# Kernel tuning notes

Hardware: AMD Instinct MI355X
Metric: run time of the kernel (lower is better)

## Reference

```python
import math
import jax, jax.numpy as jnp
import numpy as np

B, S, H, D = 8, 2048, 16, 80
DM = H * D  # 1280 = input_dims


def setup_inputs() -> dict:
    key = jax.random.key(0)
    ks = jax.random.split(key, 10)
    s = 0.02
    return {
        "x": jax.random.normal(ks[0], (B, S, DM), dtype=jnp.float32),
        "Wq": jax.random.normal(ks[1], (DM, DM), dtype=jnp.float32) * s,
        "bq": jnp.zeros((DM,), dtype=jnp.float32),
        "Wk": jax.random.normal(ks[2], (DM, DM), dtype=jnp.float32) * s,
        "bk": jnp.zeros((DM,), dtype=jnp.float32),
        "Wv": jax.random.normal(ks[3], (DM, DM), dtype=jnp.float32) * s,
        "bv": jnp.zeros((DM,), dtype=jnp.float32),
        "Wp": jax.random.normal(ks[4], (DM, DM), dtype=jnp.float32) * s,
        "bp": jnp.zeros((DM,), dtype=jnp.float32),
        "per_dim_scale": jnp.ones((D,), dtype=jnp.float32),
    }


def reference(x, Wq, bq, Wk, bk, Wv, bv, Wp, bp, per_dim_scale):
    # Projections: [B,S,DM] -> [B,S,H,D]
    q = (x @ Wq + bq).reshape(B, S, H, D)
    k = (x @ Wk + bk).reshape(B, S, H, D)
    v = (x @ Wv + bv).reshape(B, S, H, D)
    # Faithful to source: matmul over last two dims of (B,S,H,D) tensors,
    # i.e. scores are [B,S,H,H] -- mixing across HEADS at each position.
    scale = 1.0 / math.sqrt(D)
    attn = jnp.einsum('bshd,bstd->bsht', q, k) * scale  # [B,S,H,H]
    attn = jax.nn.softmax(attn, axis=-1)
    out = jnp.einsum('bsht,bstd->bshd', attn, v)  # [B,S,H,D]
    out = out * per_dim_scale  # broadcast over D
    out = out.reshape(B, S, DM)
    return out @ Wp + bp
```

## Files before the change

### kernel.cpp

```cpp
#include <hip/hip_runtime.h>
#include <hip/hip_bf16.h>

#define M_TOT   16384
#define DMODEL  1280
#define NHEAD   16
#define DHEAD   80
#define NTC     5
#define BK      64
#define NKT     (DMODEL / BK)

typedef __attribute__((ext_vector_type(8))) __bf16 bf16x8;
typedef __attribute__((ext_vector_type(4))) float  f32x4;

__device__ __forceinline__ void gload16(const void* g, void* l) {
  __builtin_amdgcn_global_load_lds(
      (const __attribute__((address_space(1))) void*)g,
      (__attribute__((address_space(3))) void*)l, 16, 0, 0);
}

__device__ __forceinline__ float bf2f(unsigned short u) {
  return __uint_as_float((unsigned)u << 16);
}

__global__ __launch_bounds__(256) void cvt_bf16_kernel(
    const float* __restrict__ x, __hip_bfloat16* __restrict__ y, int n4) {
  int i = blockIdx.x * 256 + threadIdx.x;
  if (i >= n4) return;
  float4 v = ((const float4*)x)[i];
  union { ushort4 u; __hip_bfloat16 h[4]; } o;
  o.h[0] = __float2bfloat16(v.x);
  o.h[1] = __float2bfloat16(v.y);
  o.h[2] = __float2bfloat16(v.z);
  o.h[3] = __float2bfloat16(v.w);
  ((ushort4*)y)[i] = o.u;
}

__global__ __launch_bounds__(256) void transpose_cvt_kernel(
    const float* __restrict__ W0, const float* __restrict__ W1,
    const float* __restrict__ W2, const float* __restrict__ W3,
    const float* __restrict__ pds,
    __hip_bfloat16* __restrict__ T0, __hip_bfloat16* __restrict__ T1,
    __hip_bfloat16* __restrict__ T2, __hip_bfloat16* __restrict__ T3) {
  const float* W = blockIdx.z == 0 ? W0 : blockIdx.z == 1 ? W1
                 : blockIdx.z == 2 ? W2 : W3;
  __hip_bfloat16* T = blockIdx.z == 0 ? T0 : blockIdx.z == 1 ? T1
                    : blockIdx.z == 2 ? T2 : T3;
  __shared__ float tile[32][33];
  int bx = blockIdx.x * 32, by = blockIdx.y * 32;
  int tx = threadIdx.x, ty = threadIdx.y;
  for (int j = 0; j < 32; j += 8)
    tile[ty + j][tx] = W[(size_t)(by + ty + j) * DMODEL + bx + tx];
  __syncthreads();
  const float scale = (blockIdx.z == 3) ? pds[(by + tx) % DHEAD] : 1.0f;
  for (int j = 0; j < 32; j += 8)
    T[(size_t)(bx + ty + j) * DMODEL + by + tx] =
        __float2bfloat16(tile[tx][ty + j] * scale);
}

#define MFMA16(AF, BF, MB)                                                   \
  do {                                                                       \
    _Pragma("unroll")                                                        \
    for (int j_ = 0; j_ < 4; ++j_) {                                         \
      _Pragma("unroll")                                                      \
      for (int n_ = 0; n_ < 4; ++n_)                                         \
        acc[(MB) + j_][n_] = __builtin_amdgcn_mfma_f32_16x16x32_bf16(        \
            AF[j_], BF[n_], acc[(MB) + j_][n_], 0, 0, 0);                    \
    }                                                                        \
  } while (0)

template <bool OUT_BF16>
__global__ __launch_bounds__(512, 2) void gemm_bt_kernel(
    const __hip_bfloat16* __restrict__ A,
    const __hip_bfloat16* __restrict__ Bt0,
    const __hip_bfloat16* __restrict__ Bt1,
    const __hip_bfloat16* __restrict__ Bt2,
    const float* __restrict__ bias0, const float* __restrict__ bias1,
    const float* __restrict__ bias2,
    void* __restrict__ C0, void* __restrict__ C1, void* __restrict__ C2) {
  const int mat   = blockIdx.y / NTC;
  const int ntile = blockIdx.y % NTC;
  const __hip_bfloat16* Bt = mat == 0 ? Bt0 : mat == 1 ? Bt1 : Bt2;
  const float* bias        = mat == 0 ? bias0 : mat == 1 ? bias1 : bias2;
  void* C                  = mat == 0 ? C0 : mat == 1 ? C1 : C2;

  const int bm = blockIdx.x * 256;
  const int bn = ntile * 256;

  __shared__ __align__(16) char SLDS[131072];

  const int tid  = threadIdx.x;
  const int lane = tid & 63;
  const int wid  = tid >> 6;
  const int wm   = (wid >> 2) * 128;
  const int wn   = (wid & 3) * 64;
  const int lrow = lane & 15;
  const int l4   = lane >> 4;

  const int rsub  = lane >> 2;
  const int cswz  = (lane & 3) ^ ((rsub >> 1) & 3);
  const char* gsrc[2][2][2];
#pragma unroll
  for (int i = 0; i < 2; ++i) {
    const int rA = bm + wid * 32 + i * 16 + rsub;
    const int rB = bn + wid * 32 + i * 16 + rsub;
#pragma unroll
    for (int s = 0; s < 2; ++s) {
      gsrc[0][i][s] = (const char*)A  + (size_t)rA * (DMODEL * 2) + s * 64 + cswz * 16;
      gsrc[1][i][s] = (const char*)Bt + (size_t)rB * (DMODEL * 2) + s * 64 + cswz * 16;
    }
  }

  auto issueGroup = [&](int M, int s, int nbuf, size_t koff) {
    char* d = SLDS + M * 65536 + nbuf * 32768 + s * 16384 + wid * 2048;
    gload16(gsrc[M][0][s] + koff, d);
    gload16(gsrc[M][1][s] + koff, d + 1024);
  };

  f32x4 acc[8][4];
#pragma unroll
  for (int i = 0; i < 8; ++i)
#pragma unroll
    for (int j = 0; j < 4; ++j) acc[i][j] = (f32x4){0.f, 0.f, 0.f, 0.f};

  const int swz  = ((l4 ^ ((lrow >> 1) & 3)) << 4);
  const int aOff = (wm + lrow) * 64 + swz;
  const int bOff = 65536 + (wn + lrow) * 64 + swz;

  issueGroup(0, 0, 0, 0);
  issueGroup(1, 0, 0, 0);
  issueGroup(0, 1, 0, 0);
  issueGroup(1, 1, 0, 0);
  asm volatile("s_waitcnt vmcnt(4)" ::: "memory");
  __builtin_amdgcn_s_barrier();

  bf16x8 aFa[4], aFb[4], aFc[4], aFd[4], bF0[4], bF1[4];
#pragma unroll
  for (int j = 0; j < 4; ++j)
    aFa[j] = *(const bf16x8*)(const void*)(SLDS + aOff + j * 1024);
#pragma unroll
  for (int n = 0; n < 4; ++n)
    bF0[n] = *(const bf16x8*)(const void*)(SLDS + bOff + n * 1024);
#pragma unroll
  for (int j = 0; j < 4; ++j)
    aFb[j] = *(const bf16x8*)(const void*)(SLDS + aOff + (4 + j) * 1024);

  for (int t = 0; t < NKT; ++t) {
    const int buf = t & 1, nbuf = buf ^ 1;
    const int b0 = buf << 15;
    const int n0 = nbuf << 15;
    const size_t koff = (size_t)(t + 1) * (BK * 2);
    const bool pf = (t + 1 < NKT);

    if (pf) {
      issueGroup(0, 0, nbuf, koff);
      asm volatile("s_waitcnt vmcnt(2)" ::: "memory");
    } else {
      asm volatile("s_waitcnt vmcnt(0)" ::: "memory");
    }
    __builtin_amdgcn_s_barrier();
#pragma unroll
    for (int j = 0; j < 4; ++j)
      aFc[j] = *(const bf16x8*)(const void*)(SLDS + b0 + 16384 + aOff + j * 1024);
#pragma unroll
    for (int n = 0; n < 4; ++n)
      bF1[n] = *(const bf16x8*)(const void*)(SLDS + b0 + 16384 + bOff + n * 1024);
#pragma unroll
    for (int j = 0; j < 4; ++j)
      aFd[j] = *(const bf16x8*)(const void*)(SLDS + b0 + 16384 + aOff + (4 + j) * 1024);
    if (pf) issueGroup(1, 0, nbuf, koff);
    __builtin_amdgcn_s_setprio(1);
    MFMA16(aFa, bF0, 0);
    MFMA16(aFb, bF0, 4);
    __builtin_amdgcn_s_setprio(0);

    if (pf) {
      issueGroup(0, 1, nbuf, koff);
      asm volatile("s_waitcnt vmcnt(2)" ::: "memory");
      __builtin_amdgcn_s_barrier();
#pragma unroll
      for (int j = 0; j < 4; ++j)
        aFa[j] = *(const bf16x8*)(const void*)(SLDS + n0 + aOff + j * 1024);
#pragma unroll
      for (int n = 0; n < 4; ++n)
        bF0[n] = *(const bf16x8*)(const void*)(SLDS + n0 + bOff + n * 1024);
#pragma unroll
      for (int j = 0; j < 4; ++j)
        aFb[j] = *(const bf16x8*)(const void*)(SLDS + n0 + aOff + (4 + j) * 1024);
      issueGroup(1, 1, nbuf, koff);
    }
    __builtin_amdgcn_s_setprio(1);
    MFMA16(aFc, bF1, 0);
    MFMA16(aFd, bF1, 4);
    __builtin_amdgcn_s_setprio(0);
  }

  const int rbase = l4 * 4;
#pragma unroll
  for (int mi = 0; mi < 8; ++mi) {
#pragma unroll
    for (int ni = 0; ni < 4; ++ni) {
      const int col = bn + wn + ni * 16 + lrow;
      const float b2 = bias[col];
#pragma unroll
      for (int r = 0; r < 4; ++r) {
        const int row = bm + wm + mi * 16 + rbase + r;
        const float val = acc[mi][ni][r] + b2;
        if (OUT_BF16)
          ((__hip_bfloat16*)C)[(size_t)row * DMODEL + col] = __float2bfloat16(val);
        else
          ((float*)C)[(size_t)row * DMODEL + col] = val;
      }
    }
  }
}

__global__ __launch_bounds__(256, 2) void gemm_bt128_kernel(
    const __hip_bfloat16* __restrict__ A,
    const __hip_bfloat16* __restrict__ Bt,
    const float* __restrict__ bias,
    float* __restrict__ C) {
  const int bm = blockIdx.x * 128;
  const int bn = blockIdx.y * 128;

  __shared__ __align__(16) char SLDS[65536];

  const int tid  = threadIdx.x;
  const int lane = tid & 63;
  const int wid  = tid >> 6;
  const int wm   = (wid >> 1) * 64;
  const int wn   = (wid & 1) * 64;
  const int lrow = lane & 15;
  const int l4   = lane >> 4;

  const int rsub  = lane >> 2;
  const int cswz  = (lane & 3) ^ ((rsub >> 1) & 3);
  const char* gsrc[2][2][2];
#pragma unroll
  for (int i = 0; i < 2; ++i) {
    const int rA = bm + wid * 32 + i * 16 + rsub;
    const int rB = bn + wid * 32 + i * 16 + rsub;
#pragma unroll
    for (int s = 0; s < 2; ++s) {
      gsrc[0][i][s] = (const char*)A  + (size_t)rA * (DMODEL * 2) + s * 64 + cswz * 16;
      gsrc[1][i][s] = (const char*)Bt + (size_t)rB * (DMODEL * 2) + s * 64 + cswz * 16;
    }
  }

  auto issueGroup = [&](int M, int s, int nbuf, size_t koff) {
    char* d = SLDS + M * 32768 + nbuf * 16384 + s * 8192 + wid * 2048;
    gload16(gsrc[M][0][s] + koff, d);
    gload16(gsrc[M][1][s] + koff, d + 1024);
  };

  f32x4 acc[4][4];
#pragma unroll
  for (int i = 0; i < 4; ++i)
#pragma unroll
    for (int j = 0; j < 4; ++j) acc[i][j] = (f32x4){0.f, 0.f, 0.f, 0.f};

  const int swz  = ((l4 ^ ((lrow >> 1) & 3)) << 4);
  const int aOff = (wm + lrow) * 64 + swz;
  const int bOff = 32768 + (wn + lrow) * 64 + swz;

  issueGroup(0, 0, 0, 0);
  issueGroup(1, 0, 0, 0);
  issueGroup(0, 1, 0, 0);
  issueGroup(1, 1, 0, 0);

  for (int t = 0; t < NKT; ++t) {
    const int buf = t & 1, nbuf = buf ^ 1;
    const int b0 = buf << 14;
    const size_t koff = (size_t)(t + 1) * (BK * 2);
    const bool pf = (t + 1 < NKT);

    asm volatile("s_waitcnt vmcnt(4)" ::: "memory");
    __builtin_amdgcn_s_barrier();
    bf16x8 aF[4], bF[4];
#pragma unroll
    for (int j = 0; j < 4; ++j)
      aF[j] = *(const bf16x8*)(const void*)(SLDS + b0 + aOff + j * 1024);
#pragma unroll
    for (int n = 0; n < 4; ++n)
      bF[n] = *(const bf16x8*)(const void*)(SLDS + b0 + bOff + n * 1024);
    if (pf) { issueGroup(0, 0, nbuf, koff); issueGroup(1, 0, nbuf, koff); }
    __builtin_amdgcn_sched_barrier(0);
    __builtin_amdgcn_s_setprio(1);
    MFMA16(aF, bF, 0);
    __builtin_amdgcn_s_setprio(0);
    __builtin_amdgcn_sched_barrier(0);

    if (pf) asm volatile("s_waitcnt vmcnt(4)" ::: "memory");
    else    asm volatile("s_waitcnt vmcnt(0)" ::: "memory");
    __builtin_amdgcn_s_barrier();
#pragma unroll
    for (int j = 0; j < 4; ++j)
      aF[j] = *(const bf16x8*)(const void*)(SLDS + b0 + 8192 + aOff + j * 1024);
#pragma unroll
    for (int n = 0; n < 4; ++n)
      bF[n] = *(const bf16x8*)(const void*)(SLDS + b0 + 8192 + bOff + n * 1024);
    if (pf) { issueGroup(0, 1, nbuf, koff); issueGroup(1, 1, nbuf, koff); }
    __builtin_amdgcn_sched_barrier(0);
    __builtin_amdgcn_s_setprio(1);
    MFMA16(aF, bF, 0);
    __builtin_amdgcn_s_setprio(0);
    __builtin_amdgcn_sched_barrier(0);
  }

  const int rbase = l4 * 4;
#pragma unroll
  for (int mi = 0; mi < 4; ++mi) {
#pragma unroll
    for (int ni = 0; ni < 4; ++ni) {
      const int col = bn + wn + ni * 16 + lrow;
      const float bb = bias[col];
#pragma unroll
      for (int r = 0; r < 4; ++r) {
        const int row = bm + wm + mi * 16 + rbase + r;
        C[(size_t)row * DMODEL + col] = acc[mi][ni][r] + bb;
      }
    }
  }
}

__global__ __launch_bounds__(256) void attn_kernel(
    const __hip_bfloat16* __restrict__ q, const __hip_bfloat16* __restrict__ k,
    const __hip_bfloat16* __restrict__ v,
    __hip_bfloat16* __restrict__ out) {
  const size_t base = (size_t)blockIdx.x * DMODEL;
  __shared__ float qs[16][84], ks[16][84], vs[16][84];
  __shared__ float ps[16][17];
  const int tid = threadIdx.x;

  for (int c = tid; c < 480; c += 256) {
    int matid = c / 160, idx = c - matid * 160;
    int h = idx / 10, d0 = (idx - h * 10) * 8;
    const __hip_bfloat16* src = matid == 0 ? q : matid == 1 ? k : v;
    union { bf16x8 v8; unsigned short u[8]; } uu;
    uu.v8 = *(const bf16x8*)(const void*)(src + base + (size_t)idx * 8);
    float* dst = (matid == 0 ? &qs[0][0] : matid == 1 ? &ks[0][0] : &vs[0][0]) +
                 h * 84 + d0;
#pragma unroll
    for (int j = 0; j < 8; ++j) dst[j] = bf2f(uu.u[j]);
  }
  __syncthreads();

  const int h = tid >> 4, t = tid & 15;
  float s = 0.f;
#pragma unroll
  for (int d = 0; d < DHEAD; ++d) s += qs[h][d] * ks[t][d];
  s *= 0.11180339887498948f;

  float m = s;
#pragma unroll
  for (int off = 8; off; off >>= 1) m = fmaxf(m, __shfl_xor(m, off, 16));
  float e = expf(s - m);
  float sum = e;
#pragma unroll
  for (int off = 8; off; off >>= 1) sum += __shfl_xor(sum, off, 16);
  ps[h][t] = e / sum;
  __syncthreads();

  {
    const int hh   = tid >> 4;
    const int dloc = (tid & 15) * 5;
    float o[5];
#pragma unroll
    for (int j = 0; j < 5; ++j) o[j] = 0.f;
#pragma unroll
    for (int tt = 0; tt < 16; ++tt) {
      const float p = ps[hh][tt];
#pragma unroll
      for (int j = 0; j < 5; ++j) o[j] += p * vs[tt][dloc + j];
    }
    __hip_bfloat16* ob = out + base + (size_t)hh * DHEAD + dloc;
#pragma unroll
    for (int j = 0; j < 5; ++j) ob[j] = __float2bfloat16(o[j]);
  }
}

extern "C" void kernel_launch(void* const* d_in, const int* in_sizes, int n_in,
                              void* d_out, int out_size, void* d_ws, size_t ws_size,
                              hipStream_t stream) {
  const float* x   = (const float*)d_in[0];
  const float* Wq  = (const float*)d_in[1];
  const float* bq  = (const float*)d_in[2];
  const float* Wk  = (const float*)d_in[3];
  const float* bk  = (const float*)d_in[4];
  const float* Wv  = (const float*)d_in[5];
  const float* bv  = (const float*)d_in[6];
  const float* Wp  = (const float*)d_in[7];
  const float* bp  = (const float*)d_in[8];
  const float* pds = (const float*)d_in[9];
  float* out = (float*)d_out;

  char* ws = (char*)d_ws;
  const size_t ACT = (size_t)M_TOT * DMODEL * 2;
  const size_t WT  = (size_t)DMODEL * DMODEL * 2;
  __hip_bfloat16* xbf = (__hip_bfloat16*)(ws);
  __hip_bfloat16* qbf = (__hip_bfloat16*)(ws + ACT);
  __hip_bfloat16* kbf = (__hip_bfloat16*)(ws + 2 * ACT);
  __hip_bfloat16* vbf = (__hip_bfloat16*)(ws + 3 * ACT);
  __hip_bfloat16* wtq = (__hip_bfloat16*)(ws + 4 * ACT);
  __hip_bfloat16* wtk = (__hip_bfloat16*)(ws + 4 * ACT + WT);
  __hip_bfloat16* wtv = (__hip_bfloat16*)(ws + 4 * ACT + 2 * WT);
  __hip_bfloat16* wtp = (__hip_bfloat16*)(ws + 4 * ACT + 3 * WT);
  __hip_bfloat16* attnbf = xbf;

  {
    int n4 = (M_TOT * DMODEL) / 4;
    cvt_bf16_kernel<<<n4 / 256, 256, 0, stream>>>(x, xbf, n4);
  }
  {
    dim3 g(DMODEL / 32, DMODEL / 32, 4), b(32, 8);
    transpose_cvt_kernel<<<g, b, 0, stream>>>(Wq, Wk, Wv, Wp, pds,
                                              wtq, wtk, wtv, wtp);
  }
  {
    dim3 g(M_TOT / 256, 3 * NTC);
    gemm_bt_kernel<true><<<g, 512, 0, stream>>>(
        xbf, wtq, wtk, wtv, bq, bk, bv, (void*)qbf, (void*)kbf, (void*)vbf);
  }
  attn_kernel<<<M_TOT, 256, 0, stream>>>(qbf, kbf, vbf, attnbf);
  {
    dim3 g(M_TOT / 128, DMODEL / 128);
    gemm_bt128_kernel<<<g, 256, 0, stream>>>(attnbf, wtp, bp, out);
  }
}
```

Baseline: 307.4 us.

## Restructure QKV GEMM main loop into four barrier-fenced phases; pack two rows per attention block

The QKV GEMM main loop is reorganised into four phases per K-tile. Each phase loads its own fragments from LDS, issues one global-to-LDS prefetch group, and then runs a sched_barrier/s_barrier/lgkmcnt fence before its MFMA block. This replaces the previous cross-iteration fragment preloading with a more regular, compiler-fenced schedule that uses fewer live fragment registers, at the cost of more barriers per iteration. Separately, the attention kernel now handles two token positions per 512-thread block, halving the block count and the per-block launch overhead.

```diff
diff --git a/kernel.cpp b/kernel.cpp
--- a/kernel.cpp
+++ b/kernel.cpp
@@ -68,6 +68,16 @@
     }                                                                        \
   } while (0)
 
+#define PHASE_TAIL()                                                         \
+  __builtin_amdgcn_sched_barrier(0);                                         \
+  __builtin_amdgcn_s_barrier();                                              \
+  asm volatile("s_waitcnt lgkmcnt(0)" ::: "memory");                         \
+  __builtin_amdgcn_sched_barrier(0)
+
+#define PHASE_END()                                                          \
+  __builtin_amdgcn_sched_barrier(0);                                         \
+  __builtin_amdgcn_s_barrier()
+
 template <bool OUT_BF16>
 __global__ __launch_bounds__(512, 2) void gemm_bt_kernel(
     const __hip_bfloat16* __restrict__ A,
@@ -133,65 +143,67 @@
   asm volatile("s_waitcnt vmcnt(4)" ::: "memory");
   __builtin_amdgcn_s_barrier();
 
-  bf16x8 aFa[4], aFb[4], aFc[4], aFd[4], bF0[4], bF1[4];
-#pragma unroll
-  for (int j = 0; j < 4; ++j)
-    aFa[j] = *(const bf16x8*)(const void*)(SLDS + aOff + j * 1024);
-#pragma unroll
-  for (int n = 0; n < 4; ++n)
-    bF0[n] = *(const bf16x8*)(const void*)(SLDS + bOff + n * 1024);
-#pragma unroll
-  for (int j = 0; j < 4; ++j)
-    aFb[j] = *(const bf16x8*)(const void*)(SLDS + aOff + (4 + j) * 1024);
-
   for (int t = 0; t < NKT; ++t) {
     const int buf = t & 1, nbuf = buf ^ 1;
     const int b0 = buf << 15;
-    const int n0 = nbuf << 15;
     const size_t koff = (size_t)(t + 1) * (BK * 2);
     const bool pf = (t + 1 < NKT);
 
+    bf16x8 aF[4], aG[4], bF[4];
+
+#pragma unroll
+    for (int j = 0; j < 4; ++j)
+      aF[j] = *(const bf16x8*)(const void*)(SLDS + b0 + aOff + j * 1024);
+#pragma unroll
+    for (int n = 0; n < 4; ++n)
+      bF[n] = *(const bf16x8*)(const void*)(SLDS + b0 + bOff + n * 1024);
+    if (pf) issueGroup(0, 0, nbuf, koff);
+    PHASE_TAIL();
+    __builtin_amdgcn_s_setprio(1);
+    MFMA16(aF, bF, 0);
+    __builtin_amdgcn_s_setprio(0);
+    PHASE_END();
+
+#pragma unroll
+    for (int j = 0; j < 4; ++j)
+      aG[j] = *(const bf16x8*)(const void*)(SLDS + b0 + aOff + (4 + j) * 1024);
     if (pf) {
-      issueGroup(0, 0, nbuf, koff);
-      asm volatile("s_waitcnt vmcnt(2)" ::: "memory");
+      issueGroup(1, 0, nbuf, koff);
+      asm volatile("s_waitcnt vmcnt(4)" ::: "memory");
     } else {
       asm volatile("s_waitcnt vmcnt(0)" ::: "memory");
     }
-    __builtin_amdgcn_s_barrier();
-#pragma unroll
-    for (int j = 0; j < 4; ++j)
-      aFc[j] = *(const bf16x8*)(const void*)(SLDS + b0 + 16384 + aOff + j * 1024);
+    PHASE_TAIL();
+    __builtin_amdgcn_s_setprio(1);
+    MFMA16(aG, bF, 4);
+    __builtin_amdgcn_s_setprio(0);
+    PHASE_END();
+
+#pragma unroll
+    for (int j = 0; j < 4; ++j)
+      aF[j] = *(const bf16x8*)(const void*)(SLDS + b0 + 16384 + aOff + j * 1024);
 #pragma unroll
     for (int n = 0; n < 4; ++n)
-      bF1[n] = *(const bf16x8*)(const void*)(SLDS + b0 + 16384 + bOff + n * 1024);
-#pragma unroll
-    for (int j = 0; j < 4; ++j)
-      aFd[j] = *(const bf16x8*)(const void*)(SLDS + b0 + 16384 + aOff + (4 + j) * 1024);
-    if (pf) issueGroup(1, 0, nbuf, koff);
-    __builtin_amdgcn_s_setprio(1);
-    MFMA16(aFa, bF0, 0);
-    MFMA16(aFb, bF0, 4);
-    __builtin_amdgcn_s_setprio(0);
-
+      bF[n] = *(const bf16x8*)(const void*)(SLDS + b0 + 16384 + bOff + n * 1024);
+    if (pf) issueGroup(0, 1, nbuf, koff);
+    PHASE_TAIL();
+    __builtin_amdgcn_s_setprio(1);
+    MFMA16(aF, bF, 0);
+    __builtin_amdgcn_s_setprio(0);
+    PHASE_END();
+
+#pragma unroll
+    for (int j = 0; j < 4; ++j)
+      aG[j] = *(const bf16x8*)(const void*)(SLDS + b0 + 16384 + aOff + (4 + j) * 1024);
     if (pf) {
-      issueGroup(0, 1, nbuf, koff);
-      asm volatile("s_waitcnt vmcnt(2)" ::: "memory");
-      __builtin_amdgcn_s_barrier();
-#pragma unroll
-      for (int j = 0; j < 4; ++j)
-        aFa[j] = *(const bf16x8*)(const void*)(SLDS + n0 + aOff + j * 1024);
-#pragma unroll
-      for (int n = 0; n < 4; ++n)
-        bF0[n] = *(const bf16x8*)(const void*)(SLDS + n0 + bOff + n * 1024);
-#pragma unroll
-      for (int j = 0; j < 4; ++j)
-        aFb[j] = *(const bf16x8*)(const void*)(SLDS + n0 + aOff + (4 + j) * 1024);
       issueGroup(1, 1, nbuf, koff);
-    }
-    __builtin_amdgcn_s_setprio(1);
-    MFMA16(aFc, bF1, 0);
-    MFMA16(aFd, bF1, 4);
-    __builtin_amdgcn_s_setprio(0);
+      asm volatile("s_waitcnt vmcnt(4)" ::: "memory");
+    }
+    PHASE_TAIL();
+    __builtin_amdgcn_s_setprio(1);
+    MFMA16(aG, bF, 4);
+    __builtin_amdgcn_s_setprio(0);
+    PHASE_END();
   }
 
   const int rbase = l4 * 4;
@@ -322,14 +334,15 @@
   }
 }
 
-__global__ __launch_bounds__(256) void attn_kernel(
+__global__ __launch_bounds__(512) void attn_kernel(
     const __hip_bfloat16* __restrict__ q, const __hip_bfloat16* __restrict__ k,
     const __hip_bfloat16* __restrict__ v,
     __hip_bfloat16* __restrict__ out) {
-  const size_t base = (size_t)blockIdx.x * DMODEL;
-  __shared__ float qs[16][84], ks[16][84], vs[16][84];
-  __shared__ float ps[16][17];
-  const int tid = threadIdx.x;
+  const int half = threadIdx.x >> 8;
+  const int tid  = threadIdx.x & 255;
+  const size_t base = ((size_t)blockIdx.x * 2 + half) * DMODEL;
+  __shared__ float qs[2][16][84], ks[2][16][84], vs[2][16][84];
+  __shared__ float ps[2][16][17];
 
   for (int c = tid; c < 480; c += 256) {
     int matid = c / 160, idx = c - matid * 160;
@@ -337,8 +350,8 @@
     const __hip_bfloat16* src = matid == 0 ? q : matid == 1 ? k : v;
     union { bf16x8 v8; unsigned short u[8]; } uu;
     uu.v8 = *(const bf16x8*)(const void*)(src + base + (size_t)idx * 8);
-    float* dst = (matid == 0 ? &qs[0][0] : matid == 1 ? &ks[0][0] : &vs[0][0]) +
-                 h * 84 + d0;
+    float* dst = (matid == 0 ? &qs[half][0][0] : matid == 1 ? &ks[half][0][0]
+                                               : &vs[half][0][0]) + h * 84 + d0;
 #pragma unroll
     for (int j = 0; j < 8; ++j) dst[j] = bf2f(uu.u[j]);
   }
@@ -347,7 +360,7 @@
   const int h = tid >> 4, t = tid & 15;
   float s = 0.f;
 #pragma unroll
-  for (int d = 0; d < DHEAD; ++d) s += qs[h][d] * ks[t][d];
+  for (int d = 0; d < DHEAD; ++d) s += qs[half][h][d] * ks[half][t][d];
   s *= 0.11180339887498948f;
 
   float m = s;
@@ -357,7 +370,7 @@
   float sum = e;
 #pragma unroll
   for (int off = 8; off; off >>= 1) sum += __shfl_xor(sum, off, 16);
-  ps[h][t] = e / sum;
+  ps[half][h][t] = e / sum;
   __syncthreads();
 
   {
@@ -368,9 +381,9 @@
     for (int j = 0; j < 5; ++j) o[j] = 0.f;
 #pragma unroll
     for (int tt = 0; tt < 16; ++tt) {
-      const float p = ps[hh][tt];
-#pragma unroll
-      for (int j = 0; j < 5; ++j) o[j] += p * vs[tt][dloc + j];
+      const float p = ps[half][hh][tt];
+#pragma unroll
+      for (int j = 0; j < 5; ++j) o[j] += p * vs[half][tt][dloc + j];
     }
     __hip_bfloat16* ob = out + base + (size_t)hh * DHEAD + dloc;
 #pragma unroll
@@ -420,7 +433,7 @@
     gemm_bt_kernel<true><<<g, 512, 0, stream>>>(
         xbf, wtq, wtk, wtv, bq, bk, bv, (void*)qbf, (void*)kbf, (void*)vbf);
   }
-  attn_kernel<<<M_TOT, 256, 0, stream>>>(qbf, kbf, vbf, attnbf);
+  attn_kernel<<<M_TOT / 2, 512, 0, stream>>>(qbf, kbf, vbf, attnbf);
   {
     dim3 g(M_TOT / 128, DMODEL / 128);
     gemm_bt128_kernel<<<g, 256, 0, stream>>>(attnbf, wtp, bp, out);
```

Result: no change. 312.5 us (+1.7%).
